# Performance work log

Hardware: AMD Instinct MI355X
Metric: run time of the kernel (lower is better)

The kernel has to match this reference:

```python
import jax, jax.numpy as jnp
import numpy as np

N = 100000      # nodes
E = 1600000     # edges (before self-loops)
F_IN = 128      # num_features
H = 4           # heads
C = 32          # out_channels per head (num_hidden)
SLOPE = 0.2     # leaky relu negative slope (alpha)


def setup_inputs() -> dict:
    key = jax.random.key(0)
    k = jax.random.split(key, 6)
    x = jax.random.normal(k[0], (N, F_IN), jnp.float32)
    edge_index = jax.random.randint(k[1], (2, E), 0, N, dtype=jnp.int64)
    W = jax.random.normal(k[2], (F_IN, H * C), jnp.float32) * (1.0 / np.sqrt(F_IN))
    att_src = jax.random.normal(k[3], (H, C), jnp.float32) * 0.1
    att_dst = jax.random.normal(k[4], (H, C), jnp.float32) * 0.1
    bias = jnp.zeros((H * C,), jnp.float32)
    return dict(x=x, W=W, att_src=att_src, att_dst=att_dst, bias=bias,
                edge_index=edge_index)


def reference(x, W, att_src, att_dst, bias, edge_index):
    # PyG GATConv (concat=True, add_self_loops=True), eval mode (dropout off).
    loops = jnp.arange(N, dtype=edge_index.dtype)
    ei = jnp.concatenate([edge_index, jnp.stack([loops, loops])], axis=1)
    src, dst = ei[0], ei[1]                     # [E+N]

    h = (x @ W).reshape(N, H, C)                # projected node features
    a_src = jnp.einsum('nhc,hc->nh', h, att_src)   # [N, H]
    a_dst = jnp.einsum('nhc,hc->nh', h, att_dst)   # [N, H]

    e = a_src[src] + a_dst[dst]                 # [E+N, H]
    e = jnp.where(e > 0, e, SLOPE * e)          # leaky relu

    # segment softmax over incoming edges of each dst node (per head)
    m = jax.lax.stop_gradient(jax.ops.segment_max(e, dst, num_segments=N))
    p = jnp.exp(e - m[dst])
    denom = jax.ops.segment_sum(p, dst, num_segments=N)
    alpha = p / (denom[dst] + 1e-16)            # [E+N, H]

    # weighted scatter-aggregate of source features
    out = jax.ops.segment_sum(alpha[:, :, None] * h[src], dst, num_segments=N)
    return out.reshape(N, H * C) + bias
```

## Files before the change

kernel.cpp:

```cpp
#include <hip/hip_runtime.h>
#include <hip/hip_bf16.h>
#include <math.h>

#define N_NODES 100000
#define F_IN    128
#define HC      128
#define NH      4
#define SLOPE   0.2f

#define PADK    136

#define NB      196
#define BSH     9
#define CAP     10240
#define CAPC    10752
#define CHUNK   2048
#define CURPAD  16

typedef __attribute__((ext_vector_type(8))) short short8;
typedef __attribute__((ext_vector_type(4))) float f32x4;

static __device__ __forceinline__ float leaky(float x) { return x > 0.f ? x : SLOPE * x; }

static __device__ __forceinline__ short f2bs(float f) {
    __hip_bfloat16 b = __float2bfloat16(f);
    return *reinterpret_cast<short*>(&b);
}

__global__ __launch_bounds__(256) void k_pre(const float* __restrict__ W,
                                             unsigned short* __restrict__ wt,
                                             int* __restrict__ bucket_cursor)
{
    int t = blockIdx.x * 256 + threadIdx.x;
    if (t < 128 * 128) {
        int k = t >> 7, n = t & 127;
        wt[n * 128 + k] = (unsigned short)f2bs(W[k * HC + n]);
    }
    if (t < NB * CURPAD) bucket_cursor[t] = 0;
}

__global__ __launch_bounds__(256) void k_bucket(const int* __restrict__ srcp,
                                                const int* __restrict__ dstp,
                                                int* __restrict__ bucket_cursor,
                                                int* __restrict__ eb, int E)
{
    __shared__ int ebuf[CHUNK];
    __shared__ unsigned char bkt[CHUNK];
    __shared__ int hist[256];
    __shared__ int lexcl[257];
    __shared__ int gbase[256];
    __shared__ int sdata[256];

    const int t = threadIdx.x;
    const int base = blockIdx.x * CHUNK;

    hist[t] = 0;
    __syncthreads();

    #pragma unroll
    for (int j = 0; j < CHUNK / 256; ++j) {
        int i = base + t + j * 256;
        if (i < E) atomicAdd(&hist[dstp[i] >> BSH], 1);
    }
    __syncthreads();

    int cnt = hist[t];
    sdata[t] = cnt;
    __syncthreads();
    for (int o = 1; o < 256; o <<= 1) {
        int add = (t >= o) ? sdata[t - o] : 0;
        __syncthreads();
        sdata[t] += add;
        __syncthreads();
    }
    int excl = sdata[t] - cnt;
    lexcl[t] = excl;
    if (t == 255) lexcl[256] = sdata[255];
    hist[t] = excl;
    int gb = 0;
    if (t < NB && cnt > 0) gb = atomicAdd(&bucket_cursor[t * CURPAD], cnt);
    gbase[t] = t * CAP + gb;
    __syncthreads();

    #pragma unroll
    for (int j = 0; j < CHUNK / 256; ++j) {
        int i = base + t + j * 256;
        if (i < E) {
            int s = srcp[i], d = dstp[i];
            int b = d >> BSH;
            int r = atomicAdd(&hist[b], 1);
            ebuf[r] = (s << BSH) | (d & 511);
            bkt[r] = (unsigned char)b;
        }
    }
    __syncthreads();

    const int blockTotal = lexcl[256];
    for (int i = t; i < blockTotal; i += 256) {
        int b = bkt[i];
        eb[gbase[b] + (i - lexcl[b])] = ebuf[i];
    }
}

union SMem {
    struct {
        short xs[64 * PADK];
        short ws[128 * PADK];
    } g;
    struct {
        int deg[512];
        int sdata[256];
    } c;
};

__global__ __launch_bounds__(256) void k_fused(const float* __restrict__ x,
                                               const unsigned short* __restrict__ wt,
                                               const float* __restrict__ att_src,
                                               const float* __restrict__ att_dst,
                                               unsigned short* __restrict__ hb,
                                               float* __restrict__ a_src,
                                               float* __restrict__ a_dst,
                                               const int* __restrict__ eb,
                                               const int* __restrict__ bucket_cursor,
                                               int* __restrict__ col,
                                               int2* __restrict__ rowse)
{
    __shared__ SMem sm;
    const int t = threadIdx.x;

    if (blockIdx.x < NB) {
        const int b  = blockIdx.x;
        const int n0 = b * 512;
        const int cnt   = bucket_cursor[b * CURPAD];
        const int ebase = b * CAP;
        const int gofs  = b * CAPC;

        sm.c.deg[t]       = (n0 + t       < N_NODES) ? 1 : 0;
        sm.c.deg[t + 256] = (n0 + t + 256 < N_NODES) ? 1 : 0;
        __syncthreads();

        for (int i = t; i < cnt; i += 256)
            atomicAdd(&sm.c.deg[eb[ebase + i] & 511], 1);
        __syncthreads();

        int d0 = sm.c.deg[2 * t], d1 = sm.c.deg[2 * t + 1];
        int ps = d0 + d1;
        sm.c.sdata[t] = ps;
        __syncthreads();
        for (int o = 1; o < 256; o <<= 1) {
            int add = (t >= o) ? sm.c.sdata[t - o] : 0;
            __syncthreads();
            sm.c.sdata[t] += add;
            __syncthreads();
        }
        int e0 = sm.c.sdata[t] - ps;
        int e1 = e0 + d0;
        __syncthreads();

        int na = n0 + 2 * t, nb2 = n0 + 2 * t + 1;
        if (na < N_NODES) {
            rowse[na] = make_int2(gofs + e0, gofs + e0 + d0);
            col[gofs + e0] = na;
        }
        if (nb2 < N_NODES) {
            rowse[nb2] = make_int2(gofs + e1, gofs + e1 + d1);
            col[gofs + e1] = nb2;
        }
        sm.c.deg[2 * t]     = e0 + 1;
        sm.c.deg[2 * t + 1] = e1 + 1;
        __syncthreads();

        for (int i = t; i < cnt; i += 256) {
            int v = eb[ebase + i];
            int r = atomicAdd(&sm.c.deg[v & 511], 1);
            col[gofs + r] = v >> BSH;
        }
    } else {
        const int r0 = (blockIdx.x - NB) * 64;

        for (int i = t; i < 2048; i += 256) {
            int row = i >> 5, kq = (i & 31) * 4;
            int gr = r0 + row;
            float4 v = make_float4(0.f, 0.f, 0.f, 0.f);
            if (gr < N_NODES) v = ((const float4*)(x + (size_t)gr * F_IN))[i & 31];
            short* p = &sm.g.xs[row * PADK + kq];
            p[0] = f2bs(v.x); p[1] = f2bs(v.y); p[2] = f2bs(v.z); p[3] = f2bs(v.w);
        }
        for (int i = t; i < 2048; i += 256) {
            int n = i >> 4, k0 = (i & 15) * 8;
            *(float4*)&sm.g.ws[n * PADK + k0] = *(const float4*)&wt[n * 128 + k0];
        }
        __syncthreads();

        const int wave = t >> 6, lane = t & 63;
        const int quad = lane >> 4, l16 = lane & 15;
        const int wrow = wave * 16;

        f32x4 acc[8];
        #pragma unroll
        for (int nt = 0; nt < 8; ++nt) acc[nt] = (f32x4){0.f, 0.f, 0.f, 0.f};

        const short* ap = &sm.g.xs[(wrow + l16) * PADK + quad * 8];
        #pragma unroll
        for (int kb = 0; kb < 4; ++kb) {
            short8 a = *(const short8*)(ap + kb * 32);
            #pragma unroll
            for (int nt = 0; nt < 8; ++nt) {
                short8 b = *(const short8*)&sm.g.ws[(nt * 16 + l16) * PADK + kb * 32 + quad * 8];
                acc[nt] = __builtin_amdgcn_mfma_f32_16x16x32_bf16(a, b, acc[nt], 0, 0, 0);
            }
        }

        float att_s[8], att_d[8];
        #pragma unroll
        for (int nt = 0; nt < 8; ++nt) {
            att_s[nt] = att_src[nt * 16 + l16];
            att_d[nt] = att_dst[nt * 16 + l16];
        }

        #pragma unroll
        for (int g = 0; g < 4; ++g) {
            int r = r0 + wrow + quad * 4 + g;
            if (r < N_NODES) {
                #pragma unroll
                for (int nt = 0; nt < 8; ++nt)
                    hb[(size_t)r * HC + nt * 16 + l16] = (unsigned short)f2bs(acc[nt][g]);
            }
            float s0 = acc[0][g] * att_s[0] + acc[1][g] * att_s[1];
            float s1 = acc[2][g] * att_s[2] + acc[3][g] * att_s[3];
            float s2 = acc[4][g] * att_s[4] + acc[5][g] * att_s[5];
            float s3 = acc[6][g] * att_s[6] + acc[7][g] * att_s[7];
            float d0 = acc[0][g] * att_d[0] + acc[1][g] * att_d[1];
            float d1 = acc[2][g] * att_d[2] + acc[3][g] * att_d[3];
            float d2 = acc[4][g] * att_d[4] + acc[5][g] * att_d[5];
            float d3 = acc[6][g] * att_d[6] + acc[7][g] * att_d[7];
            #pragma unroll
            for (int o = 1; o < 16; o <<= 1) {
                s0 += __shfl_xor(s0, o); s1 += __shfl_xor(s1, o);
                s2 += __shfl_xor(s2, o); s3 += __shfl_xor(s3, o);
                d0 += __shfl_xor(d0, o); d1 += __shfl_xor(d1, o);
                d2 += __shfl_xor(d2, o); d3 += __shfl_xor(d3, o);
            }
            if (l16 == 0 && r < N_NODES) {
                *(float4*)&a_src[r * NH] = make_float4(s0, s1, s2, s3);
                *(float4*)&a_dst[r * NH] = make_float4(d0, d1, d2, d3);
            }
        }
    }
}

__global__ __launch_bounds__(256) void k_node(const unsigned short* __restrict__ hb,
                                              const float* __restrict__ a_src,
                                              const float* __restrict__ a_dst,
                                              const int2* __restrict__ rowse,
                                              const int* __restrict__ col,
                                              const float* __restrict__ bias,
                                              float* __restrict__ out)
{
    const int lane = threadIdx.x & 63;
    const int node = blockIdx.x * 4 + (threadIdx.x >> 6);
    if (node >= N_NODES) return;

    const int g   = lane >> 4;
    const int l16 = lane & 15;
    const int myh = l16 >> 2;

    const int2 se = rowse[node];
    const int r0 = se.x;
    const int cnt = se.y - se.x;

    const float adm = a_dst[node * NH + myh];

    float acc[8];
    #pragma unroll
    for (int k = 0; k < 8; ++k) acc[k] = 0.f;
    float denom = 0.f;

    int i = 0;
    for (; i + 8 <= cnt; i += 8) {
        int s0 = col[r0 + i + g];
        int s1 = col[r0 + i + 4 + g];
        float as0 = a_src[s0 * NH + myh];
        float as1 = a_src[s1 * NH + myh];
        uint4 h0 = ((const uint4*)(hb + (size_t)s0 * HC))[l16];
        uint4 h1 = ((const uint4*)(hb + (size_t)s1 * HC))[l16];
        float p0 = __expf(leaky(as0 + adm));
        float p1 = __expf(leaky(as1 + adm));
        denom += p0 + p1;
        acc[0] += p0 * __uint_as_float(h0.x << 16)        + p1 * __uint_as_float(h1.x << 16);
        acc[1] += p0 * __uint_as_float(h0.x & 0xffff0000u) + p1 * __uint_as_float(h1.x & 0xffff0000u);
        acc[2] += p0 * __uint_as_float(h0.y << 16)        + p1 * __uint_as_float(h1.y << 16);
        acc[3] += p0 * __uint_as_float(h0.y & 0xffff0000u) + p1 * __uint_as_float(h1.y & 0xffff0000u);
        acc[4] += p0 * __uint_as_float(h0.z << 16)        + p1 * __uint_as_float(h1.z << 16);
        acc[5] += p0 * __uint_as_float(h0.z & 0xffff0000u) + p1 * __uint_as_float(h1.z & 0xffff0000u);
        acc[6] += p0 * __uint_as_float(h0.w << 16)        + p1 * __uint_as_float(h1.w << 16);
        acc[7] += p0 * __uint_as_float(h0.w & 0xffff0000u) + p1 * __uint_as_float(h1.w & 0xffff0000u);
    }
    for (; i < cnt; i += 4) {
        int e = i + g;
        bool v = e < cnt;
        int s = col[r0 + (v ? e : 0)];
        float as = a_src[s * NH + myh];
        uint4 h0 = ((const uint4*)(hb + (size_t)s * HC))[l16];
        float p = v ? __expf(leaky(as + adm)) : 0.f;
        denom += p;
        acc[0] += p * __uint_as_float(h0.x << 16);
        acc[1] += p * __uint_as_float(h0.x & 0xffff0000u);
        acc[2] += p * __uint_as_float(h0.y << 16);
        acc[3] += p * __uint_as_float(h0.y & 0xffff0000u);
        acc[4] += p * __uint_as_float(h0.z << 16);
        acc[5] += p * __uint_as_float(h0.z & 0xffff0000u);
        acc[6] += p * __uint_as_float(h0.w << 16);
        acc[7] += p * __uint_as_float(h0.w & 0xffff0000u);
    }

    #pragma unroll
    for (int o = 16; o < 64; o <<= 1) {
        denom += __shfl_xor(denom, o);
        #pragma unroll
        for (int k = 0; k < 8; ++k) acc[k] += __shfl_xor(acc[k], o);
    }

    if (g == 0) {
        float inv = 1.f / (denom + 1e-16f);
        const float* bp = &bias[l16 * 8];
        f32x4 o0, o1;
        o0.x = acc[0] * inv + bp[0]; o0.y = acc[1] * inv + bp[1];
        o0.z = acc[2] * inv + bp[2]; o0.w = acc[3] * inv + bp[3];
        o1.x = acc[4] * inv + bp[4]; o1.y = acc[5] * inv + bp[5];
        o1.z = acc[6] * inv + bp[6]; o1.w = acc[7] * inv + bp[7];
        __builtin_nontemporal_store(o0, (f32x4*)&out[(size_t)node * HC + l16 * 8]);
        __builtin_nontemporal_store(o1, (f32x4*)&out[(size_t)node * HC + l16 * 8 + 4]);
    }
}

extern "C" void kernel_launch(void* const* d_in, const int* in_sizes, int n_in,
                              void* d_out, int out_size, void* d_ws, size_t ws_size,
                              hipStream_t stream)
{
    const float* x       = (const float*)d_in[0];
    const float* W       = (const float*)d_in[1];
    const float* att_src = (const float*)d_in[2];
    const float* att_dst = (const float*)d_in[3];
    const float* bias    = (const float*)d_in[4];
    const int*   ei      = (const int*)d_in[5];
    const int E = in_sizes[5] / 2;
    const int* srcp = ei;
    const int* dstp = ei + E;
    float* out = (float*)d_out;

    char* wsb = (char*)d_ws;
    size_t off = 0;
    auto alloc = [&](size_t bytes) -> char* {
        char* p = wsb + off;
        off += (bytes + 255) & ~(size_t)255;
        return p;
    };
    unsigned short* hb = (unsigned short*)alloc((size_t)N_NODES * HC * sizeof(unsigned short));
    float* a_src   = (float*)alloc((size_t)N_NODES * NH * sizeof(float));
    float* a_dst   = (float*)alloc((size_t)N_NODES * NH * sizeof(float));
    int*   eb      = (int*)alloc((size_t)NB * CAP * sizeof(int));
    int*   col     = (int*)alloc((size_t)NB * CAPC * sizeof(int));
    int2*  rowse   = (int2*)alloc((size_t)N_NODES * sizeof(int2));
    int*   bcursor = (int*)alloc((size_t)NB * CURPAD * sizeof(int));
    unsigned short* wt = (unsigned short*)alloc(128 * 128 * sizeof(unsigned short));

    const int bucketBlocks = (E + CHUNK - 1) / CHUNK;
    const int gemmBlocks   = (N_NODES + 63) / 64;

    k_pre<<<64, 256, 0, stream>>>(W, wt, bcursor);
    k_bucket<<<bucketBlocks, 256, 0, stream>>>(srcp, dstp, bcursor, eb, E);
    k_fused<<<NB + gemmBlocks, 256, 0, stream>>>(x, wt, att_src, att_dst,
                                                 hb, a_src, a_dst,
                                                 eb, bcursor, col, rowse);
    k_node<<<(N_NODES + 3) / 4, 256, 0, stream>>>(hb, a_src, a_dst, rowse, col, bias, out);
}
```

Before: 247.4 us.

## Fold attention vectors into W, stream GEMM operands, prefetch gathers in aggregation

Precomputes W·att_src and W·att_dst as an extra bf16 MFMA tile so the attention logits come out of the GEMM, replacing per-row shuffle reductions. The GEMM now reads x and W directly from global memory instead of staging them in LDS, and stages the bf16 output through LDS for coalesced stores. Bucketing keeps the edge src/dst in registers instead of reloading them. The node aggregation loop is software-pipelined over 16 edges with prefetched col and feature gathers and packed fp32 FMAs, with the col array zero-padded so the prefetch stays in bounds. Risks include bf16 rounding of the folded attention weights and higher register pressure.

```diff
diff --git a/kernel.cpp b/kernel.cpp
--- a/kernel.cpp
+++ b/kernel.cpp
@@ -7,8 +7,6 @@
 #define HC      128
 #define NH      4
 #define SLOPE   0.2f
-
-#define PADK    136
 
 #define NB      196
 #define BSH     9
@@ -19,6 +17,7 @@
 
 typedef __attribute__((ext_vector_type(8))) short short8;
 typedef __attribute__((ext_vector_type(4))) float f32x4;
+typedef __attribute__((ext_vector_type(2))) float fx2;
 
 static __device__ __forceinline__ float leaky(float x) { return x > 0.f ? x : SLOPE * x; }
 
@@ -27,14 +26,37 @@
     return *reinterpret_cast<short*>(&b);
 }
 
+static __device__ __forceinline__ fx2 bf2f2(unsigned int v) {
+    fx2 r;
+    r.x = __uint_as_float(v << 16);
+    r.y = __uint_as_float(v & 0xffff0000u);
+    return r;
+}
+
 __global__ __launch_bounds__(256) void k_pre(const float* __restrict__ W,
+                                             const float* __restrict__ att_src,
+                                             const float* __restrict__ att_dst,
                                              unsigned short* __restrict__ wt,
+                                             unsigned short* __restrict__ wab,
                                              int* __restrict__ bucket_cursor)
 {
     int t = blockIdx.x * 256 + threadIdx.x;
     if (t < 128 * 128) {
         int k = t >> 7, n = t & 127;
         wt[n * 128 + k] = (unsigned short)f2bs(W[k * HC + n]);
+    } else if (t < 17408) {
+        int i = t - 16384;
+        int k = i >> 3, slot = i & 7;
+        int head = slot & 3;
+        const float* av = (slot & 4) ? att_dst : att_src;
+        float dot = 0.f;
+        #pragma unroll
+        for (int c = 0; c < 32; ++c)
+            dot += W[k * HC + head * 32 + c] * av[head * 32 + c];
+        wab[slot * 128 + k] = (unsigned short)f2bs(dot);
+    } else if (t < 18432) {
+        int i = t - 17408;
+        wab[(8 + (i >> 7)) * 128 + (i & 127)] = 0;
     }
     if (t < NB * CURPAD) bucket_cursor[t] = 0;
 }
@@ -57,10 +79,14 @@
     hist[t] = 0;
     __syncthreads();
 
+    int sreg[8], dreg[8];
     #pragma unroll
     for (int j = 0; j < CHUNK / 256; ++j) {
         int i = base + t + j * 256;
-        if (i < E) atomicAdd(&hist[dstp[i] >> BSH], 1);
+        bool v = i < E;
+        sreg[j] = v ? srcp[i] : 0;
+        dreg[j] = v ? dstp[i] : -1;
+        if (v) atomicAdd(&hist[dreg[j] >> BSH], 1);
     }
     __syncthreads();
 
@@ -84,12 +110,10 @@
 
     #pragma unroll
     for (int j = 0; j < CHUNK / 256; ++j) {
-        int i = base + t + j * 256;
-        if (i < E) {
-            int s = srcp[i], d = dstp[i];
-            int b = d >> BSH;
+        if (dreg[j] >= 0) {
+            int b = dreg[j] >> BSH;
             int r = atomicAdd(&hist[b], 1);
-            ebuf[r] = (s << BSH) | (d & 511);
+            ebuf[r] = (sreg[j] << BSH) | (dreg[j] & 511);
             bkt[r] = (unsigned char)b;
         }
     }
@@ -103,10 +127,7 @@
 }
 
 union SMem {
-    struct {
-        short xs[64 * PADK];
-        short ws[128 * PADK];
-    } g;
+    short ob[64 * 128];
     struct {
         int deg[512];
         int sdata[256];
@@ -115,8 +136,7 @@
 
 __global__ __launch_bounds__(256) void k_fused(const float* __restrict__ x,
                                                const unsigned short* __restrict__ wt,
-                                               const float* __restrict__ att_src,
-                                               const float* __restrict__ att_dst,
+                                               const unsigned short* __restrict__ wab,
                                                unsigned short* __restrict__ hb,
                                                float* __restrict__ a_src,
                                                float* __restrict__ a_dst,
@@ -134,9 +154,10 @@
         const int cnt   = bucket_cursor[b * CURPAD];
         const int ebase = b * CAP;
         const int gofs  = b * CAPC;
-
-        sm.c.deg[t]       = (n0 + t       < N_NODES) ? 1 : 0;
-        sm.c.deg[t + 256] = (n0 + t + 256 < N_NODES) ? 1 : 0;
+        const int nvalid = min(512, N_NODES - n0);
+
+        sm.c.deg[t]       = (t       < nvalid) ? 1 : 0;
+        sm.c.deg[t + 256] = (t + 256 < nvalid) ? 1 : 0;
         __syncthreads();
 
         for (int i = t; i < cnt; i += 256)
@@ -175,76 +196,62 @@
             int r = atomicAdd(&sm.c.deg[v & 511], 1);
             col[gofs + r] = v >> BSH;
         }
+        const int top = cnt + nvalid;
+        const int upper = min(CAPC, (top + 64 + 15) & ~15);
+        for (int i = top + t; i < upper; i += 256) col[gofs + i] = 0;
     } else {
         const int r0 = (blockIdx.x - NB) * 64;
-
-        for (int i = t; i < 2048; i += 256) {
-            int row = i >> 5, kq = (i & 31) * 4;
-            int gr = r0 + row;
-            float4 v = make_float4(0.f, 0.f, 0.f, 0.f);
-            if (gr < N_NODES) v = ((const float4*)(x + (size_t)gr * F_IN))[i & 31];
-            short* p = &sm.g.xs[row * PADK + kq];
-            p[0] = f2bs(v.x); p[1] = f2bs(v.y); p[2] = f2bs(v.z); p[3] = f2bs(v.w);
-        }
-        for (int i = t; i < 2048; i += 256) {
-            int n = i >> 4, k0 = (i & 15) * 8;
-            *(float4*)&sm.g.ws[n * PADK + k0] = *(const float4*)&wt[n * 128 + k0];
-        }
-        __syncthreads();
-
         const int wave = t >> 6, lane = t & 63;
         const int quad = lane >> 4, l16 = lane & 15;
         const int wrow = wave * 16;
 
+        const int grow = r0 + wrow + l16;
+        const int xrow = min(grow, N_NODES - 1);
+        const float* xp = x + (size_t)xrow * F_IN;
+
         f32x4 acc[8];
         #pragma unroll
         for (int nt = 0; nt < 8; ++nt) acc[nt] = (f32x4){0.f, 0.f, 0.f, 0.f};
-
-        const short* ap = &sm.g.xs[(wrow + l16) * PADK + quad * 8];
+        f32x4 acca = (f32x4){0.f, 0.f, 0.f, 0.f};
+
         #pragma unroll
         for (int kb = 0; kb < 4; ++kb) {
-            short8 a = *(const short8*)(ap + kb * 32);
+            float4 xa = *(const float4*)&xp[kb * 32 + quad * 8];
+            float4 xb = *(const float4*)&xp[kb * 32 + quad * 8 + 4];
+            short8 a;
+            a[0] = f2bs(xa.x); a[1] = f2bs(xa.y); a[2] = f2bs(xa.z); a[3] = f2bs(xa.w);
+            a[4] = f2bs(xb.x); a[5] = f2bs(xb.y); a[6] = f2bs(xb.z); a[7] = f2bs(xb.w);
             #pragma unroll
             for (int nt = 0; nt < 8; ++nt) {
-                short8 b = *(const short8*)&sm.g.ws[(nt * 16 + l16) * PADK + kb * 32 + quad * 8];
+                short8 b = *(const short8*)&wt[(nt * 16 + l16) * 128 + kb * 32 + quad * 8];
                 acc[nt] = __builtin_amdgcn_mfma_f32_16x16x32_bf16(a, b, acc[nt], 0, 0, 0);
             }
-        }
-
-        float att_s[8], att_d[8];
-        #pragma unroll
-        for (int nt = 0; nt < 8; ++nt) {
-            att_s[nt] = att_src[nt * 16 + l16];
-            att_d[nt] = att_dst[nt * 16 + l16];
+            short8 bwa = *(const short8*)&wab[l16 * 128 + kb * 32 + quad * 8];
+            acca = __builtin_amdgcn_mfma_f32_16x16x32_bf16(a, bwa, acca, 0, 0, 0);
         }
 
         #pragma unroll
         for (int g = 0; g < 4; ++g) {
-            int r = r0 + wrow + quad * 4 + g;
+            int lrow = wrow + quad * 4 + g;
+            int r = r0 + lrow;
+            #pragma unroll
+            for (int nt = 0; nt < 8; ++nt)
+                sm.ob[lrow * 128 + nt * 16 + l16] = f2bs(acc[nt][g]);
             if (r < N_NODES) {
-                #pragma unroll
-                for (int nt = 0; nt < 8; ++nt)
-                    hb[(size_t)r * HC + nt * 16 + l16] = (unsigned short)f2bs(acc[nt][g]);
+                if (l16 < 4)      a_src[r * NH + l16]       = acca[g];
+                else if (l16 < 8) a_dst[r * NH + (l16 - 4)] = acca[g];
             }
-            float s0 = acc[0][g] * att_s[0] + acc[1][g] * att_s[1];
-            float s1 = acc[2][g] * att_s[2] + acc[3][g] * att_s[3];
-            float s2 = acc[4][g] * att_s[4] + acc[5][g] * att_s[5];
-            float s3 = acc[6][g] * att_s[6] + acc[7][g] * att_s[7];
-            float d0 = acc[0][g] * att_d[0] + acc[1][g] * att_d[1];
-            float d1 = acc[2][g] * att_d[2] + acc[3][g] * att_d[3];
-            float d2 = acc[4][g] * att_d[4] + acc[5][g] * att_d[5];
-            float d3 = acc[6][g] * att_d[6] + acc[7][g] * att_d[7];
-            #pragma unroll
-            for (int o = 1; o < 16; o <<= 1) {
-                s0 += __shfl_xor(s0, o); s1 += __shfl_xor(s1, o);
-                s2 += __shfl_xor(s2, o); s3 += __shfl_xor(s3, o);
-                d0 += __shfl_xor(d0, o); d1 += __shfl_xor(d1, o);
-                d2 += __shfl_xor(d2, o); d3 += __shfl_xor(d3, o);
-            }
-            if (l16 == 0 && r < N_NODES) {
-                *(float4*)&a_src[r * NH] = make_float4(s0, s1, s2, s3);
-                *(float4*)&a_dst[r * NH] = make_float4(d0, d1, d2, d3);
-            }
+        }
+        __syncthreads();
+
+        const int4* s4 = (const int4*)sm.ob;
+        #pragma unroll
+        for (int i = 0; i < 4; ++i) {
+            int c = i * 256 + t;
+            int row = c >> 4;
+            int r = r0 + row;
+            if (r < N_NODES)
+                *(int4*)&hb[(size_t)r * HC + (c & 15) * 8] = s4[c];
         }
     }
 }
@@ -271,64 +278,76 @@
 
     const float adm = a_dst[node * NH + myh];
 
-    float acc[8];
+    fx2 acc2[4];
     #pragma unroll
-    for (int k = 0; k < 8; ++k) acc[k] = 0.f;
+    for (int k = 0; k < 4; ++k) acc2[k] = (fx2){0.f, 0.f};
     float denom = 0.f;
 
-    int i = 0;
-    for (; i + 8 <= cnt; i += 8) {
-        int s0 = col[r0 + i + g];
-        int s1 = col[r0 + i + 4 + g];
-        float as0 = a_src[s0 * NH + myh];
-        float as1 = a_src[s1 * NH + myh];
-        uint4 h0 = ((const uint4*)(hb + (size_t)s0 * HC))[l16];
-        uint4 h1 = ((const uint4*)(hb + (size_t)s1 * HC))[l16];
-        float p0 = __expf(leaky(as0 + adm));
-        float p1 = __expf(leaky(as1 + adm));
-        denom += p0 + p1;
-        acc[0] += p0 * __uint_as_float(h0.x << 16)        + p1 * __uint_as_float(h1.x << 16);
-        acc[1] += p0 * __uint_as_float(h0.x & 0xffff0000u) + p1 * __uint_as_float(h1.x & 0xffff0000u);
-        acc[2] += p0 * __uint_as_float(h0.y << 16)        + p1 * __uint_as_float(h1.y << 16);
-        acc[3] += p0 * __uint_as_float(h0.y & 0xffff0000u) + p1 * __uint_as_float(h1.y & 0xffff0000u);
-        acc[4] += p0 * __uint_as_float(h0.z << 16)        + p1 * __uint_as_float(h1.z << 16);
-        acc[5] += p0 * __uint_as_float(h0.z & 0xffff0000u) + p1 * __uint_as_float(h1.z & 0xffff0000u);
-        acc[6] += p0 * __uint_as_float(h0.w << 16)        + p1 * __uint_as_float(h1.w << 16);
-        acc[7] += p0 * __uint_as_float(h0.w & 0xffff0000u) + p1 * __uint_as_float(h1.w & 0xffff0000u);
-    }
-    for (; i < cnt; i += 4) {
-        int e = i + g;
-        bool v = e < cnt;
-        int s = col[r0 + (v ? e : 0)];
-        float as = a_src[s * NH + myh];
-        uint4 h0 = ((const uint4*)(hb + (size_t)s * HC))[l16];
-        float p = v ? __expf(leaky(as + adm)) : 0.f;
-        denom += p;
-        acc[0] += p * __uint_as_float(h0.x << 16);
-        acc[1] += p * __uint_as_float(h0.x & 0xffff0000u);
-        acc[2] += p * __uint_as_float(h0.y << 16);
-        acc[3] += p * __uint_as_float(h0.y & 0xffff0000u);
-        acc[4] += p * __uint_as_float(h0.z << 16);
-        acc[5] += p * __uint_as_float(h0.z & 0xffff0000u);
-        acc[6] += p * __uint_as_float(h0.w << 16);
-        acc[7] += p * __uint_as_float(h0.w & 0xffff0000u);
-    }
+    #define HROW(c) (((const uint4*)(hb + (size_t)(c) * HC))[l16])
+
+    int   c0 = col[r0 + g],      c1 = col[r0 + 4 + g];
+    int   c2 = col[r0 + 8 + g],  c3 = col[r0 + 12 + g];
+    float a0 = a_src[c0 * NH + myh], a1 = a_src[c1 * NH + myh];
+    float a2 = a_src[c2 * NH + myh], a3 = a_src[c3 * NH + myh];
+    uint4 h0 = HROW(c0), h1 = HROW(c1), h2 = HROW(c2), h3 = HROW(c3);
+    int   n0 = col[r0 + 16 + g], n1 = col[r0 + 20 + g];
+    int   n2 = col[r0 + 24 + g], n3 = col[r0 + 28 + g];
+
+    for (int i = 0; i < cnt; i += 16) {
+        float b0 = a_src[n0 * NH + myh], b1 = a_src[n1 * NH + myh];
+        float b2 = a_src[n2 * NH + myh], b3 = a_src[n3 * NH + myh];
+        uint4 j0 = HROW(n0), j1 = HROW(n1), j2 = HROW(n2), j3 = HROW(n3);
+        int m0 = col[r0 + i + 32 + g], m1 = col[r0 + i + 36 + g];
+        int m2 = col[r0 + i + 40 + g], m3 = col[r0 + i + 44 + g];
+
+        float p0 = (i + g      < cnt) ? __expf(leaky(a0 + adm)) : 0.f;
+        float p1 = (i + 4 + g  < cnt) ? __expf(leaky(a1 + adm)) : 0.f;
+        float p2 = (i + 8 + g  < cnt) ? __expf(leaky(a2 + adm)) : 0.f;
+        float p3 = (i + 12 + g < cnt) ? __expf(leaky(a3 + adm)) : 0.f;
+        denom += (p0 + p1) + (p2 + p3);
+        fx2 q0 = (fx2){p0, p0}, q1 = (fx2){p1, p1};
+        fx2 q2 = (fx2){p2, p2}, q3 = (fx2){p3, p3};
+        acc2[0] = __builtin_elementwise_fma(bf2f2(h0.x), q0, acc2[0]);
+        acc2[0] = __builtin_elementwise_fma(bf2f2(h1.x), q1, acc2[0]);
+        acc2[0] = __builtin_elementwise_fma(bf2f2(h2.x), q2, acc2[0]);
+        acc2[0] = __builtin_elementwise_fma(bf2f2(h3.x), q3, acc2[0]);
+        acc2[1] = __builtin_elementwise_fma(bf2f2(h0.y), q0, acc2[1]);
+        acc2[1] = __builtin_elementwise_fma(bf2f2(h1.y), q1, acc2[1]);
+        acc2[1] = __builtin_elementwise_fma(bf2f2(h2.y), q2, acc2[1]);
+        acc2[1] = __builtin_elementwise_fma(bf2f2(h3.y), q3, acc2[1]);
+        acc2[2] = __builtin_elementwise_fma(bf2f2(h0.z), q0, acc2[2]);
+        acc2[2] = __builtin_elementwise_fma(bf2f2(h1.z), q1, acc2[2]);
+        acc2[2] = __builtin_elementwise_fma(bf2f2(h2.z), q2, acc2[2]);
+        acc2[2] = __builtin_elementwise_fma(bf2f2(h3.z), q3, acc2[2]);
+        acc2[3] = __builtin_elementwise_fma(bf2f2(h0.w), q0, acc2[3]);
+        acc2[3] = __builtin_elementwise_fma(bf2f2(h1.w), q1, acc2[3]);
+        acc2[3] = __builtin_elementwise_fma(bf2f2(h2.w), q2, acc2[3]);
+        acc2[3] = __builtin_elementwise_fma(bf2f2(h3.w), q3, acc2[3]);
+
+        a0 = b0; a1 = b1; a2 = b2; a3 = b3;
+        h0 = j0; h1 = j1; h2 = j2; h3 = j3;
+        n0 = m0; n1 = m1; n2 = m2; n3 = m3;
+    }
+    #undef HROW
 
     #pragma unroll
     for (int o = 16; o < 64; o <<= 1) {
         denom += __shfl_xor(denom, o);
         #pragma unroll
-        for (int k = 0; k < 8; ++k) acc[k] += __shfl_xor(acc[k], o);
+        for (int k = 0; k < 4; ++k) {
+            acc2[k].x += __shfl_xor(acc2[k].x, o);
+            acc2[k].y += __shfl_xor(acc2[k].y, o);
+        }
     }
 
     if (g == 0) {
         float inv = 1.f / (denom + 1e-16f);
         const float* bp = &bias[l16 * 8];
         f32x4 o0, o1;
-        o0.x = acc[0] * inv + bp[0]; o0.y = acc[1] * inv + bp[1];
-        o0.z = acc[2] * inv + bp[2]; o0.w = acc[3] * inv + bp[3];
-        o1.x = acc[4] * inv + bp[4]; o1.y = acc[5] * inv + bp[5];
-        o1.z = acc[6] * inv + bp[6]; o1.w = acc[7] * inv + bp[7];
+        o0.x = acc2[0].x * inv + bp[0]; o0.y = acc2[0].y * inv + bp[1];
+        o0.z = acc2[1].x * inv + bp[2]; o0.w = acc2[1].y * inv + bp[3];
+        o1.x = acc2[2].x * inv + bp[4]; o1.y = acc2[2].y * inv + bp[5];
+        o1.z = acc2[3].x * inv + bp[6]; o1.w = acc2[3].y * inv + bp[7];
         __builtin_nontemporal_store(o0, (f32x4*)&out[(size_t)node * HC + l16 * 8]);
         __builtin_nontemporal_store(o1, (f32x4*)&out[(size_t)node * HC + l16 * 8 + 4]);
     }
@@ -363,15 +382,15 @@
     int*   col     = (int*)alloc((size_t)NB * CAPC * sizeof(int));
     int2*  rowse   = (int2*)alloc((size_t)N_NODES * sizeof(int2));
     int*   bcursor = (int*)alloc((size_t)NB * CURPAD * sizeof(int));
-    unsigned short* wt = (unsigned short*)alloc(128 * 128 * sizeof(unsigned short));
+    unsigned short* wt  = (unsigned short*)alloc(128 * 128 * sizeof(unsigned short));
+    unsigned short* wab = (unsigned short*)alloc(16 * 128 * sizeof(unsigned short));
 
     const int bucketBlocks = (E + CHUNK - 1) / CHUNK;
     const int gemmBlocks   = (N_NODES + 63) / 64;
 
-    k_pre<<<64, 256, 0, stream>>>(W, wt, bcursor);
+    k_pre<<<73, 256, 0, stream>>>(W, att_src, att_dst, wt, wab, bcursor);
     k_bucket<<<bucketBlocks, 256, 0, stream>>>(srcp, dstp, bcursor, eb, E);
-    k_fused<<<NB + gemmBlocks, 256, 0, stream>>>(x, wt, att_src, att_dst,
-                                                 hb, a_src, a_dst,
+    k_fused<<<NB + gemmBlocks, 256, 0, stream>>>(x, wt, wab, hb, a_src, a_dst,
                                                  eb, bcursor, col, rowse);
     k_node<<<(N_NODES + 3) / 4, 256, 0, stream>>>(hb, a_src, a_dst, rowse, col, bias, out);
 }
```

Result: slower. 253.9 us (+2.6%).
